# Kernel optimization log

Hardware: AMD Instinct MI355X
Metric: run time of the kernel (lower is better)

Reference implementation:

```python
import jax, jax.numpy as jnp
import numpy as np

B, H, S, DH = 2, 16, 2048, 64
MASK_FILL = -10000.0


def setup_inputs() -> dict:
    key = jax.random.key(0)
    kq, kk, kv = jax.random.split(key, 3)
    q = jax.random.normal(kq, (B, H, S, DH), dtype=jnp.float32)
    k = jax.random.normal(kk, (B, H, S, DH), dtype=jnp.float32)
    v = jax.random.normal(kv, (B, H, S, DH), dtype=jnp.float32)
    # causal mask: True where attention is disallowed (upper triangle)
    mask = jnp.triu(jnp.ones((S, S), dtype=jnp.bool_), k=1)
    return {"q": q, "k": k, "v": v, "mask": mask}


def reference(q, k, v, mask):
    scale = 1.0 / jnp.sqrt(jnp.asarray(k.shape[-1], dtype=q.dtype))
    # scores: [B, H, S_q, S_k]
    scores = jnp.einsum("bhqd,bhkd->bhqk", q, k) * scale
    # additive mask: masked_fill on a zeros [S_k, S_v] matrix -> -10000 where mask
    attn_bias = jnp.where(mask, jnp.asarray(MASK_FILL, dtype=k.dtype),
                          jnp.asarray(0.0, dtype=k.dtype))
    scores = scores + attn_bias  # broadcast over batch/heads
    attn = jax.nn.softmax(scores, axis=-1)
    # dropout_rate = 0.0 -> identity
    return jnp.einsum("bhqk,bhkd->bhqd", attn, v)
```

## Files before the change

kernel.cpp:

```cpp
#include <hip/hip_runtime.h>


#define S_LEN  2048
#define DHDIM  64
#define NHEADS 32
#define LDP    72
#define M2     23.083120654223414f
#define QSCALE 0.18033688011117658f

typedef __attribute__((ext_vector_type(8))) short bf16x8;
typedef __attribute__((ext_vector_type(4))) float f32x4;

__device__ __forceinline__ unsigned short f2bf(float f) {
    unsigned u = __float_as_uint(f);
    return (unsigned short)((u + 0x7fffu + ((u >> 16) & 1u)) >> 16);
}
__device__ __forceinline__ float bf2f(unsigned short b) {
    return __uint_as_float(((unsigned)b) << 16);
}
__device__ __forceinline__ void ld8(const float* p, float* f) {
    float4 a = *(const float4*)p, b = *(const float4*)(p + 4);
    f[0]=a.x; f[1]=a.y; f[2]=a.z; f[3]=a.w; f[4]=b.x; f[5]=b.y; f[6]=b.z; f[7]=b.w;
}
__device__ __forceinline__ uint4 pack8(const float* f, float scale) {
    union { uint4 v; unsigned short s[8]; } w;
    #pragma unroll
    for (int j = 0; j < 8; j++) w.s[j] = f2bf(f[j] * scale);
    return w.v;
}

__global__ __launch_bounds__(256) void prep(
    const float* __restrict__ Qf, const float* __restrict__ Kf,
    const float* __restrict__ Vf, unsigned short* __restrict__ qb,
    unsigned short* __restrict__ kb, unsigned short* __restrict__ vtb)
{
    const int st = blockIdx.x, bh = blockIdx.y;
    __shared__ unsigned short lt[64][LDP];
    const float* vp = Vf + ((size_t)bh * S_LEN + st * 64) * DHDIM;
    for (int c = threadIdx.x; c < 512; c += 256) {
        int s = c >> 3, d0 = (c & 7) * 8;
        float f[8]; ld8(vp + s * DHDIM + d0, f);
        #pragma unroll
        for (int j = 0; j < 8; j++) lt[d0 + j][s] = f2bf(f[j]);
    }
    size_t off = ((size_t)(bh * 32 + st) * 4096) + (size_t)threadIdx.x * 16;
    float f[8];
    ld8(Qf + off, f);     *(uint4*)(qb + off)     = pack8(f, QSCALE);
    ld8(Qf + off + 8, f); *(uint4*)(qb + off + 8) = pack8(f, QSCALE);
    ld8(Kf + off, f);     *(uint4*)(kb + off)     = pack8(f, 1.0f);
    ld8(Kf + off + 8, f); *(uint4*)(kb + off + 8) = pack8(f, 1.0f);
    __syncthreads();
    unsigned short* op = vtb + (size_t)bh * DHDIM * S_LEN + st * 64;
    for (int c = threadIdx.x; c < 512; c += 256) {
        int d = c >> 3, s0 = (c & 7) * 8;
        *(uint4*)(op + (size_t)d * S_LEN + s0) = *(const uint4*)&lt[d][s0];
    }
}

template <bool PRE>
__global__ __launch_bounds__(256) void fattn_kernel(
    const void* __restrict__ Qp, const void* __restrict__ Kp,
    const void* __restrict__ Vp, float* __restrict__ O)
{
    __shared__ unsigned short qs[64][LDP];
    __shared__ unsigned short ks[64][LDP];
    __shared__ unsigned short vts[64][LDP];
    __shared__ unsigned short ps[4][16][LDP];

    const int id = blockIdx.y * 32 + blockIdx.x;
    const int g  = id >> 8;
    const int r8 = id & 255;
    const int bh = r8 >> 3;
    const int s  = r8 & 7;
    const int qt = (g == 0) ? 31 - 2 * s
                 : (g == 1) ? 2 * s
                 : (g == 2) ? 30 - 2 * s
                            : 2 * s + 1;

    const int tid = threadIdx.x;
    const int wave = tid >> 6, lane = tid & 63;
    const int quad = lane >> 4, l16 = lane & 15;
    const int qrow = wave * 16 + quad * 4;

    if constexpr (PRE) {
        const unsigned short* src = (const unsigned short*)Qp
            + ((size_t)bh * S_LEN + qt * 64) * DHDIM;
        for (int c = tid; c < 512; c += 256) {
            int row = c >> 3, c8 = (c & 7) * 8;
            *(uint4*)&qs[row][c8] = *(const uint4*)(src + row * DHDIM + c8);
        }
    } else {
        const float* src = (const float*)Qp + ((size_t)bh * S_LEN + qt * 64) * DHDIM;
        for (int c = tid; c < 512; c += 256) {
            int row = c >> 3, c8 = (c & 7) * 8;
            float f[8]; ld8(src + row * DHDIM + c8, f);
            *(uint4*)&qs[row][c8] = pack8(f, QSCALE);
        }
    }
    __syncthreads();

    const bf16x8 aq0 = *(const bf16x8*)&qs[wave * 16 + l16][quad * 8];
    const bf16x8 aq1 = *(const bf16x8*)&qs[wave * 16 + l16][32 + quad * 8];

    float l_p[4];
    f32x4 of[4];
    #pragma unroll
    for (int r = 0; r < 4; r++) l_p[r] = 0.f;
    #pragma unroll
    for (int n = 0; n < 4; n++) of[n] = (f32x4){0.f, 0.f, 0.f, 0.f};

    for (int kt = 0; kt <= qt; kt++) {
        __syncthreads();

        if constexpr (PRE) {
            const unsigned short* ksrc = (const unsigned short*)Kp
                + ((size_t)bh * S_LEN + kt * 64) * DHDIM;
            const unsigned short* vsrc = (const unsigned short*)Vp
                + (size_t)bh * DHDIM * S_LEN + kt * 64;
            for (int c = tid; c < 512; c += 256) {
                int row = c >> 3, c8 = (c & 7) * 8;
                *(uint4*)&ks[row][c8]  = *(const uint4*)(ksrc + row * DHDIM + c8);
                *(uint4*)&vts[row][c8] = *(const uint4*)(vsrc + (size_t)row * S_LEN + c8);
            }
        } else {
            const float* ksrc = (const float*)Kp + ((size_t)bh * S_LEN + kt * 64) * DHDIM;
            const float* vsrc = (const float*)Vp + ((size_t)bh * S_LEN + kt * 64) * DHDIM;
            for (int c = tid; c < 512; c += 256) {
                int row = c >> 3, c8 = (c & 7) * 8;
                float f[8];
                ld8(ksrc + row * DHDIM + c8, f);
                *(uint4*)&ks[row][c8] = pack8(f, 1.0f);
                ld8(vsrc + row * DHDIM + c8, f);
                #pragma unroll
                for (int j = 0; j < 8; j++) vts[c8 + j][row] = f2bf(f[j]);
            }
        }
        __syncthreads();

        f32x4 sf[4];
        #pragma unroll
        for (int n = 0; n < 4; n++) {
            bf16x8 b0 = *(const bf16x8*)&ks[n * 16 + l16][quad * 8];
            bf16x8 b1 = *(const bf16x8*)&ks[n * 16 + l16][32 + quad * 8];
            sf[n] = (f32x4){0.f, 0.f, 0.f, 0.f};
            sf[n] = __builtin_amdgcn_mfma_f32_16x16x32_bf16(aq0, b0, sf[n], 0, 0, 0);
            sf[n] = __builtin_amdgcn_mfma_f32_16x16x32_bf16(aq1, b1, sf[n], 0, 0, 0);
        }

        const bool diag = (kt == qt);
        #pragma unroll
        for (int n = 0; n < 4; n++) {
            int col = n * 16 + l16;
            #pragma unroll
            for (int r = 0; r < 4; r++) {
                float p = exp2f(sf[n][r] - M2);
                if (diag && col > qrow + r) p = 0.f;
                unsigned short pb = (unsigned short)(__float_as_uint(p) >> 16);
                l_p[r] += bf2f(pb);
                ps[wave][quad * 4 + r][col] = pb;
            }
        }
        asm volatile("s_waitcnt lgkmcnt(0)" ::: "memory");

        bf16x8 ap0 = *(const bf16x8*)&ps[wave][l16][quad * 8];
        bf16x8 ap1 = *(const bf16x8*)&ps[wave][l16][32 + quad * 8];
        #pragma unroll
        for (int n = 0; n < 4; n++) {
            bf16x8 bv0 = *(const bf16x8*)&vts[n * 16 + l16][quad * 8];
            bf16x8 bv1 = *(const bf16x8*)&vts[n * 16 + l16][32 + quad * 8];
            of[n] = __builtin_amdgcn_mfma_f32_16x16x32_bf16(ap0, bv0, of[n], 0, 0, 0);
            of[n] = __builtin_amdgcn_mfma_f32_16x16x32_bf16(ap1, bv1, of[n], 0, 0, 0);
        }
    }

    float* op = O + ((size_t)bh * S_LEN + qt * 64) * DHDIM;
    #pragma unroll
    for (int r = 0; r < 4; r++) {
        float l = l_p[r];
        l += __shfl_xor(l, 1);
        l += __shfl_xor(l, 2);
        l += __shfl_xor(l, 4);
        l += __shfl_xor(l, 8);
        float inv = 1.f / l;
        int row = qrow + r;
        #pragma unroll
        for (int n = 0; n < 4; n++)
            op[row * DHDIM + n * 16 + l16] = of[n][r] * inv;
    }
}

extern "C" void kernel_launch(void* const* d_in, const int* in_sizes, int n_in,
                              void* d_out, int out_size, void* d_ws, size_t ws_size,
                              hipStream_t stream) {
    const float* Q = (const float*)d_in[0];
    const float* K = (const float*)d_in[1];
    const float* V = (const float*)d_in[2];
    float* O = (float*)d_out;
    const size_t N = (size_t)NHEADS * S_LEN * DHDIM;

    if (ws_size >= 3 * N * sizeof(unsigned short) && d_ws) {
        unsigned short* qb  = (unsigned short*)d_ws;
        unsigned short* kb  = qb + N;
        unsigned short* vtb = kb + N;
        prep<<<dim3(S_LEN / 64, NHEADS), 256, 0, stream>>>(Q, K, V, qb, kb, vtb);
        fattn_kernel<true><<<dim3(32, 32), 256, 0, stream>>>(qb, kb, vtb, O);
    } else {
        fattn_kernel<false><<<dim3(32, 32), 256, 0, stream>>>(Q, K, V, O);
    }
}
```

Measured before the change: 160.3 us.

## Transpose MFMA operands so each lane owns a query row; reuse Q smem for P

Swaps the MFMA operand order so scores and outputs come out transposed, with each lane holding one query row's values. This lets P be written as packed 64-bit stores via byte-permute and lets the output be written as float4. The row-sum reduction shrinks to two shuffles, and the max offset is folded into the accumulator init. The P tile now reuses the Q shared buffer, cutting LDS footprint, and the row sum now accumulates unrounded fp32 p instead of the bf16-truncated values fed to the MFMA.

Measured after the change: 158.6 us. Within noise of the previous version (-1.0%).

```diff
diff --git a/kernel.cpp b/kernel.cpp
--- a/kernel.cpp
+++ b/kernel.cpp
@@ -15,9 +15,6 @@
     unsigned u = __float_as_uint(f);
     return (unsigned short)((u + 0x7fffu + ((u >> 16) & 1u)) >> 16);
 }
-__device__ __forceinline__ float bf2f(unsigned short b) {
-    return __uint_as_float(((unsigned)b) << 16);
-}
 __device__ __forceinline__ void ld8(const float* p, float* f) {
     float4 a = *(const float4*)p, b = *(const float4*)(p + 4);
     f[0]=a.x; f[1]=a.y; f[2]=a.z; f[3]=a.w; f[4]=b.x; f[5]=b.y; f[6]=b.z; f[7]=b.w;
@@ -27,6 +24,13 @@
     #pragma unroll
     for (int j = 0; j < 8; j++) w.s[j] = f2bf(f[j] * scale);
     return w.v;
+}
+__device__ __forceinline__ unsigned packhi(float a, float b) {
+#if __has_builtin(__builtin_amdgcn_perm)
+    return __builtin_amdgcn_perm(__float_as_uint(b), __float_as_uint(a), 0x07060302u);
+#else
+    return (__float_as_uint(a) >> 16) | (__float_as_uint(b) & 0xffff0000u);
+#endif
 }
 
 __global__ __launch_bounds__(256) void prep(
@@ -62,25 +66,25 @@
     const void* __restrict__ Qp, const void* __restrict__ Kp,
     const void* __restrict__ Vp, float* __restrict__ O)
 {
-    __shared__ unsigned short qs[64][LDP];
-    __shared__ unsigned short ks[64][LDP];
-    __shared__ unsigned short vts[64][LDP];
-    __shared__ unsigned short ps[4][16][LDP];
+    __shared__ unsigned short smem[192 * LDP];
+    unsigned short (*ks)[LDP]  = (unsigned short(*)[LDP])smem;
+    unsigned short (*vts)[LDP] = (unsigned short(*)[LDP])(smem + 64 * LDP);
+    unsigned short (*qs)[LDP]  = (unsigned short(*)[LDP])(smem + 128 * LDP);
+    unsigned short (*pst)[LDP] = qs;
 
     const int id = blockIdx.y * 32 + blockIdx.x;
     const int g  = id >> 8;
     const int r8 = id & 255;
     const int bh = r8 >> 3;
-    const int s  = r8 & 7;
-    const int qt = (g == 0) ? 31 - 2 * s
-                 : (g == 1) ? 2 * s
-                 : (g == 2) ? 30 - 2 * s
-                            : 2 * s + 1;
+    const int s8 = r8 & 7;
+    const int qt = (g == 0) ? 31 - 2 * s8
+                 : (g == 1) ? 2 * s8
+                 : (g == 2) ? 30 - 2 * s8
+                            : 2 * s8 + 1;
 
     const int tid = threadIdx.x;
     const int wave = tid >> 6, lane = tid & 63;
     const int quad = lane >> 4, l16 = lane & 15;
-    const int qrow = wave * 16 + quad * 4;
 
     if constexpr (PRE) {
         const unsigned short* src = (const unsigned short*)Qp
@@ -99,13 +103,12 @@
     }
     __syncthreads();
 
-    const bf16x8 aq0 = *(const bf16x8*)&qs[wave * 16 + l16][quad * 8];
-    const bf16x8 aq1 = *(const bf16x8*)&qs[wave * 16 + l16][32 + quad * 8];
-
-    float l_p[4];
+    const int prow = wave * 16 + l16;
+    const bf16x8 bq0 = *(const bf16x8*)&qs[prow][quad * 8];
+    const bf16x8 bq1 = *(const bf16x8*)&qs[prow][32 + quad * 8];
+
+    float l_p = 0.f;
     f32x4 of[4];
-    #pragma unroll
-    for (int r = 0; r < 4; r++) l_p[r] = 0.f;
     #pragma unroll
     for (int n = 0; n < 4; n++) of[n] = (f32x4){0.f, 0.f, 0.f, 0.f};
 
@@ -140,52 +143,50 @@
         f32x4 sf[4];
         #pragma unroll
         for (int n = 0; n < 4; n++) {
-            bf16x8 b0 = *(const bf16x8*)&ks[n * 16 + l16][quad * 8];
-            bf16x8 b1 = *(const bf16x8*)&ks[n * 16 + l16][32 + quad * 8];
-            sf[n] = (f32x4){0.f, 0.f, 0.f, 0.f};
-            sf[n] = __builtin_amdgcn_mfma_f32_16x16x32_bf16(aq0, b0, sf[n], 0, 0, 0);
-            sf[n] = __builtin_amdgcn_mfma_f32_16x16x32_bf16(aq1, b1, sf[n], 0, 0, 0);
+            bf16x8 ak0 = *(const bf16x8*)&ks[n * 16 + l16][quad * 8];
+            bf16x8 ak1 = *(const bf16x8*)&ks[n * 16 + l16][32 + quad * 8];
+            sf[n] = (f32x4){-M2, -M2, -M2, -M2};
+            sf[n] = __builtin_amdgcn_mfma_f32_16x16x32_bf16(ak0, bq0, sf[n], 0, 0, 0);
+            sf[n] = __builtin_amdgcn_mfma_f32_16x16x32_bf16(ak1, bq1, sf[n], 0, 0, 0);
         }
 
         const bool diag = (kt == qt);
         #pragma unroll
         for (int n = 0; n < 4; n++) {
-            int col = n * 16 + l16;
+            float p[4];
             #pragma unroll
             for (int r = 0; r < 4; r++) {
-                float p = exp2f(sf[n][r] - M2);
-                if (diag && col > qrow + r) p = 0.f;
-                unsigned short pb = (unsigned short)(__float_as_uint(p) >> 16);
-                l_p[r] += bf2f(pb);
-                ps[wave][quad * 4 + r][col] = pb;
+                p[r] = exp2f(sf[n][r]);
+                if (diag && (n * 16 + quad * 4 + r > wave * 16 + l16)) p[r] = 0.f;
+                l_p += p[r];
             }
+            uint2 dw;
+            dw.x = packhi(p[0], p[1]);
+            dw.y = packhi(p[2], p[3]);
+            *(uint2*)&pst[prow][n * 16 + quad * 4] = dw;
         }
         asm volatile("s_waitcnt lgkmcnt(0)" ::: "memory");
 
-        bf16x8 ap0 = *(const bf16x8*)&ps[wave][l16][quad * 8];
-        bf16x8 ap1 = *(const bf16x8*)&ps[wave][l16][32 + quad * 8];
+        bf16x8 bp0 = *(const bf16x8*)&pst[prow][quad * 8];
+        bf16x8 bp1 = *(const bf16x8*)&pst[prow][32 + quad * 8];
         #pragma unroll
         for (int n = 0; n < 4; n++) {
-            bf16x8 bv0 = *(const bf16x8*)&vts[n * 16 + l16][quad * 8];
-            bf16x8 bv1 = *(const bf16x8*)&vts[n * 16 + l16][32 + quad * 8];
-            of[n] = __builtin_amdgcn_mfma_f32_16x16x32_bf16(ap0, bv0, of[n], 0, 0, 0);
-            of[n] = __builtin_amdgcn_mfma_f32_16x16x32_bf16(ap1, bv1, of[n], 0, 0, 0);
-        }
-    }
-
-    float* op = O + ((size_t)bh * S_LEN + qt * 64) * DHDIM;
+            bf16x8 av0 = *(const bf16x8*)&vts[n * 16 + l16][quad * 8];
+            bf16x8 av1 = *(const bf16x8*)&vts[n * 16 + l16][32 + quad * 8];
+            of[n] = __builtin_amdgcn_mfma_f32_16x16x32_bf16(av0, bp0, of[n], 0, 0, 0);
+            of[n] = __builtin_amdgcn_mfma_f32_16x16x32_bf16(av1, bp1, of[n], 0, 0, 0);
+        }
+    }
+
+    l_p += __shfl_xor(l_p, 16);
+    l_p += __shfl_xor(l_p, 32);
+    const float inv = 1.f / l_p;
+    float* op = O + ((size_t)bh * S_LEN + qt * 64 + wave * 16 + l16) * DHDIM;
     #pragma unroll
-    for (int r = 0; r < 4; r++) {
-        float l = l_p[r];
-        l += __shfl_xor(l, 1);
-        l += __shfl_xor(l, 2);
-        l += __shfl_xor(l, 4);
-        l += __shfl_xor(l, 8);
-        float inv = 1.f / l;
-        int row = qrow + r;
-        #pragma unroll
-        for (int n = 0; n < 4; n++)
-            op[row * DHDIM + n * 16 + l16] = of[n][r] * inv;
+    for (int n = 0; n < 4; n++) {
+        float4 o4 = make_float4(of[n][0] * inv, of[n][1] * inv,
+                                of[n][2] * inv, of[n][3] * inv);
+        *(float4*)(op + n * 16 + quad * 4) = o4;
     }
 }
 
```
